# Optimization experiments

Hardware: AMD Instinct MI355X
Metric: run time of the kernel (lower is better)

The kernel has to match this reference:

```python
import jax, jax.numpy as jnp
import numpy as np

BATCH, SEQ = 4, 2048
D_MODEL, D_STATE, D_CONV, HEADDIM = 512, 128, 4, 64
D_INNER = 1024          # expand * d_model
NHEADS = 16             # d_inner / headdim
CONV_DIM = D_INNER + 2 * D_STATE   # 1280 (ngroups=1)
D_IN_PROJ = 2 * D_INNER + 2 * D_STATE + NHEADS  # 2320


def setup_inputs() -> dict:
    key = jax.random.key(0)
    ks = jax.random.split(key, 7)
    x = jax.random.normal(ks[0], (BATCH, SEQ, D_MODEL), jnp.float32)
    norm_weight = jnp.ones((D_MODEL,), jnp.float32)
    in_proj_w = jax.random.normal(ks[1], (D_IN_PROJ, D_MODEL), jnp.float32) * 0.02
    conv_w = jax.random.normal(ks[2], (CONV_DIM, 1, D_CONV), jnp.float32) * 0.2
    conv_b = jnp.zeros((CONV_DIM,), jnp.float32)
    dt_bias = jax.random.normal(ks[3], (NHEADS,), jnp.float32) * 0.1
    A_log = jnp.log(jax.random.uniform(ks[4], (NHEADS,), jnp.float32, 1.0, 16.0))
    D_param = jnp.ones((NHEADS,), jnp.float32)
    gated_norm_weight = jnp.ones((D_INNER,), jnp.float32)
    out_proj_w = jax.random.normal(ks[5], (D_MODEL, D_INNER), jnp.float32) * 0.02
    return dict(x=x, norm_weight=norm_weight, in_proj_w=in_proj_w, conv_w=conv_w,
                conv_b=conv_b, dt_bias=dt_bias, A_log=A_log, D_param=D_param,
                gated_norm_weight=gated_norm_weight, out_proj_w=out_proj_w)


def _rmsnorm(x, w, eps):
    return w * (x * jax.lax.rsqrt(jnp.mean(x * x, axis=-1, keepdims=True) + eps))


def _mamba2_forward(x, norm_weight, in_proj_w, conv_w, conv_b, dt_bias,
                    A_log, D_param, gated_norm_weight, out_proj_w):
    b, l, _ = x.shape
    u = _rmsnorm(x, norm_weight, 1e-6)                       # pre-norm (eps=1e-6)
    zxbcdt = u @ in_proj_w.T                                 # (b,l,2320)
    z = zxbcdt[..., :D_INNER]                                # gate
    xBC = zxbcdt[..., D_INNER:D_INNER + CONV_DIM]            # (b,l,1280)
    dt = zxbcdt[..., D_INNER + CONV_DIM:]                    # (b,l,nheads)
    dt = jax.nn.softplus(dt + dt_bias)

    # causal depthwise conv1d over time + SiLU
    conv = jax.lax.conv_general_dilated(
        xBC.transpose(0, 2, 1), conv_w, window_strides=(1,),
        padding=[(D_CONV - 1, 0)], feature_group_count=CONV_DIM,
        dimension_numbers=('NCH', 'OIH', 'NCH'))
    xBC = jax.nn.silu((conv + conv_b[None, :, None]).transpose(0, 2, 1))

    xs = xBC[..., :D_INNER].reshape(b, l, NHEADS, HEADDIM)   # (b,l,h,p)
    Bmat = xBC[..., D_INNER:D_INNER + D_STATE]               # (b,l,n)
    Cmat = xBC[..., D_INNER + D_STATE:]                      # (b,l,n)

    A = -jnp.exp(A_log)                                      # (h,)
    dA = jnp.exp(dt * A)                                     # (b,l,h)
    dtx = dt[..., None] * xs                                 # (b,l,h,p)

    def step(h, inp):
        dA_t, dtx_t, B_t, C_t = inp                          # (b,h),(b,h,p),(b,n),(b,n)
        h = h * dA_t[..., None, None] + dtx_t[..., None] * B_t[:, None, None, :]
        y = jnp.einsum('bhpn,bn->bhp', h, C_t)
        return h, y

    h0 = jnp.zeros((b, NHEADS, HEADDIM, D_STATE), x.dtype)
    _, ys = jax.lax.scan(step, h0, (dA.transpose(1, 0, 2), dtx.transpose(1, 0, 2, 3),
                                    Bmat.transpose(1, 0, 2), Cmat.transpose(1, 0, 2)))
    y = ys.transpose(1, 0, 2, 3) + xs * D_param[None, None, :, None]  # D skip
    y = y.reshape(b, l, D_INNER)

    y = _rmsnorm(y * jax.nn.silu(z), gated_norm_weight, 1e-5)  # RMSNormGated (eps=1e-5)
    return x + y @ out_proj_w.T                                # residual


def reference(x, norm_weight, in_proj_w, conv_w, conv_b, dt_bias,
              A_log, D_param, gated_norm_weight, out_proj_w):
    return _mamba2_forward(x, norm_weight, in_proj_w, conv_w, conv_b, dt_bias,
                           A_log, D_param, gated_norm_weight, out_proj_w)
```

## Files before the change

kernel.cpp:

```cpp
#include <hip/hip_runtime.h>
#include <cstdint>
#include <cstddef>

#define B_ 4
#define L_ 2048
#define DMODEL 512
#define DINNER 1024
#define DSTATE 128
#define NH 16
#define HD 64
#define CONVDIM 1280
#define NPROJ 2320
#define NPAD 2432
#define ML (B_*L_)
#define Q_ 64
#define NCH 32

typedef __bf16 bf16x8 __attribute__((ext_vector_type(8)));
typedef float f32x4 __attribute__((ext_vector_type(4)));
typedef float f32x16 __attribute__((ext_vector_type(16)));

__device__ __forceinline__ float bf2f(ushort u) {
  union { unsigned int i; float f; } v; v.i = ((unsigned int)u) << 16; return v.f;
}
__device__ __forceinline__ ushort f2bf(float f) {
  union { float f; unsigned int i; } v; v.f = f;
  unsigned int u = v.i;
  unsigned int r = (u + 0x7fffu + ((u >> 16) & 1u)) >> 16;
  return (ushort)r;
}
__device__ __forceinline__ float siluf(float x) { return x / (1.f + __expf(-x)); }

__device__ __forceinline__ void gl_lds16(const void* g, void* l) {
  __builtin_amdgcn_global_load_lds(
      (const __attribute__((address_space(1))) unsigned int*)g,
      (__attribute__((address_space(3))) unsigned int*)l,
      16, 0, 0);
}

__global__ __launch_bounds__(256) void k_cvt(const float* __restrict__ wi, const float* __restrict__ wo,
                                             ushort* __restrict__ oi, ushort* __restrict__ oo) {
  int idx = blockIdx.x * 256 + threadIdx.x;
  const int n1 = NPAD * DMODEL;
  if (idx < n1) {
    int n = idx / DMODEL, k = idx % DMODEL;
    oi[idx] = f2bf((n < NPROJ) ? wi[(size_t)n * DMODEL + k] : 0.f);
  } else {
    int j = idx - n1;
    if (j < DMODEL * DINNER) oo[j] = f2bf(wo[j]);
  }
}

__global__ __launch_bounds__(256) void k_rmsnorm(const float* __restrict__ x, const float* __restrict__ w,
                                                 ushort* __restrict__ u) {
  int row = blockIdx.x * 4 + (threadIdx.x >> 6);
  int lane = threadIdx.x & 63;
  const float* xr = x + (size_t)row * DMODEL + lane * 8;
  float4 a = *(const float4*)xr;
  float4 b = *(const float4*)(xr + 4);
  float ss = a.x*a.x + a.y*a.y + a.z*a.z + a.w*a.w + b.x*b.x + b.y*b.y + b.z*b.z + b.w*b.w;
  ss += __shfl_xor(ss, 1);  ss += __shfl_xor(ss, 2);  ss += __shfl_xor(ss, 4);
  ss += __shfl_xor(ss, 8);  ss += __shfl_xor(ss, 16); ss += __shfl_xor(ss, 32);
  float sc = rsqrtf(ss * (1.f / DMODEL) + 1e-6f);
  const float* wr = w + lane * 8;
  float4 wa = *(const float4*)wr;
  float4 wb = *(const float4*)(wr + 4);
  union { ushort s[8]; int4 v; } o;
  o.s[0] = f2bf(a.x * wa.x * sc); o.s[1] = f2bf(a.y * wa.y * sc);
  o.s[2] = f2bf(a.z * wa.z * sc); o.s[3] = f2bf(a.w * wa.w * sc);
  o.s[4] = f2bf(b.x * wb.x * sc); o.s[5] = f2bf(b.y * wb.y * sc);
  o.s[6] = f2bf(b.z * wb.z * sc); o.s[7] = f2bf(b.w * wb.w * sc);
  *(int4*)(u + (size_t)row * DMODEL + lane * 8) = o.v;
}

template <int EPI, int BM, int BN, int MR, int NR>
__global__ __launch_bounds__(256) void gemm_bt(const ushort* __restrict__ A, const ushort* __restrict__ Bm,
                                               void* __restrict__ Cout, const float* __restrict__ resid,
                                               int M, int N, int K, int gx) {
  constexpr int WM = MR * 32, WN = NR * 32;
  constexpr int WAVES_N = BN / WN;
  constexpr int CH_A = BM / 8, CH_B = BN / 8;
  constexpr int PER_A = CH_A / 4, PER_B = CH_B / 4;
  constexpr int SL = PER_A + PER_B;
  __shared__ __align__(16) ushort lA[2][BM * 64];
  __shared__ __align__(16) ushort lB[2][BN * 64];
  const int nwg = gridDim.x;
  const int cpx = nwg >> 3;
  const int bid = blockIdx.x;
  const int swz = (bid & 7) * cpx + (bid >> 3);
  const int n0 = (swz % gx) * BN, m0 = (swz / gx) * BM;
  const int t = threadIdx.x;
  const int wave = t >> 6, lane = t & 63;
  const int wr = wave / WAVES_N, wc = wave % WAVES_N;
  const int r3 = lane >> 3;
  const int ce = (((lane & 7) ^ r3) << 3);
  const int nt = K >> 6;
  f32x16 acc[MR][NR] = {};
  auto stage = [&](int buf, int k0) {
#pragma unroll
    for (int i = 0; i < PER_A; ++i) {
      int chunk = wave * PER_A + i;
      int row = chunk * 8 + r3;
      gl_lds16(A + (size_t)(m0 + row) * K + k0 + ce, (char*)&lA[buf][0] + chunk * 1024);
    }
#pragma unroll
    for (int i = 0; i < PER_B; ++i) {
      int chunk = wave * PER_B + i;
      int row = chunk * 8 + r3;
      gl_lds16(Bm + (size_t)(n0 + row) * K + k0 + ce, (char*)&lB[buf][0] + chunk * 1024);
    }
  };
  stage(0, 0);
  const int rsel = lane & 31;
  const int khi = (lane >> 5) << 3;
  const int kswz = (lane & 7) << 3;
  for (int kt = 0; kt < nt; ++kt) {
    const int cur = kt & 1;
    if (kt + 1 < nt) {
      stage(cur ^ 1, (kt + 1) << 6);
      if constexpr (SL == 8) asm volatile("s_waitcnt vmcnt(8)" ::: "memory");
      else if constexpr (SL == 6) asm volatile("s_waitcnt vmcnt(6)" ::: "memory");
      else asm volatile("s_waitcnt vmcnt(0)" ::: "memory");
    } else {
      asm volatile("s_waitcnt vmcnt(0)" ::: "memory");
    }
    __builtin_amdgcn_s_barrier();
#pragma unroll
    for (int kk = 0; kk < 64; kk += 16) {
      const int kcol = (kk + khi) ^ kswz;
      bf16x8 af[MR], bfr[NR];
#pragma unroll
      for (int m = 0; m < MR; ++m)
        af[m] = *reinterpret_cast<const bf16x8*>(&lA[cur][(wr * WM + m * 32 + rsel) * 64 + kcol]);
#pragma unroll
      for (int n = 0; n < NR; ++n)
        bfr[n] = *reinterpret_cast<const bf16x8*>(&lB[cur][(wc * WN + n * 32 + rsel) * 64 + kcol]);
#pragma unroll
      for (int m = 0; m < MR; ++m)
#pragma unroll
        for (int n = 0; n < NR; ++n)
          acc[m][n] = __builtin_amdgcn_mfma_f32_32x32x16_bf16(af[m], bfr[n], acc[m][n], 0, 0, 0);
    }
    __builtin_amdgcn_s_barrier();
  }
  const int coln = lane & 31;
  const int rbase = (lane >> 5) << 2;
#pragma unroll
  for (int m = 0; m < MR; ++m) {
#pragma unroll
    for (int n = 0; n < NR; ++n) {
      int gm0 = m0 + wr * WM + m * 32 + rbase;
      int gn = n0 + wc * WN + n * 32 + coln;
#pragma unroll
      for (int r = 0; r < 16; ++r) {
        int gm = gm0 + (r & 3) + 8 * (r >> 2);
        float v = acc[m][n][r];
        if (EPI == 0) {
          ((ushort*)Cout)[(size_t)gm * N + gn] = f2bf(v);
        } else {
          ((float*)Cout)[(size_t)gm * N + gn] = v + resid[(size_t)gm * N + gn];
        }
      }
    }
  }
}

__global__ __launch_bounds__(256) void k_dtcum(const ushort* __restrict__ zx, const float* __restrict__ dt_bias,
                                               const float* __restrict__ A_log, float* __restrict__ dtb,
                                               float* __restrict__ acum) {
  int gid = blockIdx.x * 4 + (threadIdx.x >> 6);
  int lane = threadIdx.x & 63;
  int c = gid & 31, h = (gid >> 5) & 15, b = gid >> 9;
  int row = b * L_ + c * Q_ + lane;
  float raw = bf2f(zx[(size_t)row * NPAD + DINNER + CONVDIM + h]) + dt_bias[h];
  float dtv = raw > 20.f ? raw : log1pf(expf(raw));
  dtb[(size_t)row * NH + h] = dtv;
  float a = dtv * (-__expf(A_log[h]));
#pragma unroll
  for (int d = 1; d < 64; d <<= 1) {
    float o = __shfl_up(a, d);
    if (lane >= d) a += o;
  }
  acum[(size_t)row * NH + h] = a;
}

__global__ __launch_bounds__(256) void k_conv(const ushort* __restrict__ zx, const float* __restrict__ cw,
                                              const float* __restrict__ cb, ushort* __restrict__ out) {
  int t = blockIdx.x * 256 + threadIdx.x;
  int cg = t % 160;
  int rb = t / 160;
  int c0 = cg * 8;
  int l0 = (rb & 255) * 8;
  int b = rb >> 8;
  float w0[8], w1[8], w2[8], w3[8], bias[8];
#pragma unroll
  for (int j = 0; j < 8; ++j) {
    float4 wv = *(const float4*)(cw + (c0 + j) * 4);
    w0[j] = wv.x; w1[j] = wv.y; w2[j] = wv.z; w3[j] = wv.w;
    bias[j] = cb[c0 + j];
  }
  const ushort* base = zx + (size_t)(b * L_ + l0) * NPAD + DINNER + c0;
  ushort* ob = out + (size_t)(b * L_ + l0) * CONVDIM + c0;
  union U8 { int4 v; ushort s[8]; };
  float h0[8], h1[8], h2[8];
  if (l0 >= 3) {
    U8 a, bb, cc;
    a.v  = *(const int4*)(base - 3 * NPAD);
    bb.v = *(const int4*)(base - 2 * NPAD);
    cc.v = *(const int4*)(base - 1 * NPAD);
#pragma unroll
    for (int j = 0; j < 8; ++j) { h0[j] = bf2f(a.s[j]); h1[j] = bf2f(bb.s[j]); h2[j] = bf2f(cc.s[j]); }
  } else {
#pragma unroll
    for (int j = 0; j < 8; ++j) { h0[j] = 0.f; h1[j] = 0.f; h2[j] = 0.f; }
  }
#pragma unroll
  for (int i = 0; i < 8; ++i) {
    U8 xv, ov;
    xv.v = *(const int4*)(base + (size_t)i * NPAD);
#pragma unroll
    for (int j = 0; j < 8; ++j) {
      float xc = bf2f(xv.s[j]);
      float v = w0[j] * h0[j] + w1[j] * h1[j] + w2[j] * h2[j] + w3[j] * xc + bias[j];
      ov.s[j] = f2bf(siluf(v));
      h0[j] = h1[j]; h1[j] = h2[j]; h2[j] = xc;
    }
    *(int4*)(ob + (size_t)i * CONVDIM) = ov.v;
  }
}

__global__ __launch_bounds__(256) void k_state(const ushort* __restrict__ xbc, const float* __restrict__ dtb,
                                               const float* __restrict__ acum, ushort* __restrict__ Sbuf) {
  __shared__ __align__(16) ushort sBTW[128 * 72];
  __shared__ __align__(16) ushort sXT[64 * 72];
  __shared__ float sDt[64], sCum[64];
  const int blk = blockIdx.x;
  const int c = blk & 31, h = (blk >> 5) & 15, b = blk >> 9;
  const int row0 = b * L_ + c * Q_;
  const int tid = threadIdx.x;
  const int wave = tid >> 6, lane = tid & 63;
  if (tid < 64) {
    sDt[tid]  = dtb[(size_t)(row0 + tid) * NH + h];
    sCum[tid] = acum[(size_t)(row0 + tid) * NH + h];
  }
  __syncthreads();
  const float T = sCum[63];
#pragma unroll
  for (int i = 0; i < 4; ++i) {
    int idx = i * 256 + tid;
    int r = idx >> 4, n8 = (idx & 15) * 8;
    union { int4 v; ushort s[8]; } bv;
    bv.v = *(const int4*)(xbc + (size_t)(row0 + r) * CONVDIM + DINNER + n8);
    float w = sDt[r] * __expf(T - sCum[r]);
#pragma unroll
    for (int j = 0; j < 8; ++j)
      sBTW[(n8 + j) * 72 + r] = f2bf(bf2f(bv.s[j]) * w);
  }
#pragma unroll
  for (int i = 0; i < 2; ++i) {
    int idx = i * 256 + tid;
    int r = idx >> 3, p8 = (idx & 7) * 8;
    union { int4 v; ushort s[8]; } xv;
    xv.v = *(const int4*)(xbc + (size_t)(row0 + r) * CONVDIM + h * HD + p8);
#pragma unroll
    for (int j = 0; j < 8; ++j) sXT[(p8 + j) * 72 + r] = xv.s[j];
  }
  __syncthreads();
  const int rsel = lane & 15;
  const int t0 = wave * 16;
  f32x4 sa[8] = {};
#pragma unroll
  for (int k0 = 0; k0 < 64; k0 += 32) {
    int ksel = k0 + ((lane >> 4) << 3);
    bf16x8 af = *(const bf16x8*)&sXT[(t0 + rsel) * 72 + ksel];
#pragma unroll
    for (int n = 0; n < 8; ++n) {
      bf16x8 bf_ = *(const bf16x8*)&sBTW[(n * 16 + rsel) * 72 + ksel];
      sa[n] = __builtin_amdgcn_mfma_f32_16x16x32_bf16(af, bf_, sa[n], 0, 0, 0);
    }
  }
  ushort* Sp = Sbuf + (size_t)((b * NH + h) * NCH + c) * (HD * DSTATE);
  int prow = t0 + ((lane >> 4) << 2);
#pragma unroll
  for (int n = 0; n < 8; ++n) {
    int nc = n * 16 + (lane & 15);
#pragma unroll
    for (int r = 0; r < 4; ++r)
      Sp[(prow + r) * DSTATE + nc] = f2bf(sa[n][r]);
  }
}

__global__ __launch_bounds__(256) void k_scan2(ushort* __restrict__ Sbuf, const float* __restrict__ acum) {
  const int blk = blockIdx.x;
  const int ps = blk & 3, bh = blk >> 2;
  const int b = bh >> 4, h = bh & 15;
  const int off = ps * 2048 + threadIdx.x * 8;
  ushort* base = Sbuf + (size_t)bh * NCH * (HD * DSTATE) + off;
  float alphas[NCH];
#pragma unroll
  for (int c = 0; c < NCH; ++c)
    alphas[c] = __expf(acum[(size_t)(b * L_ + c * Q_ + 63) * NH + h]);
  union U8 { int4 v; ushort s[8]; };
  U8 pf[4];
#pragma unroll
  for (int i = 0; i < 4; ++i) pf[i].v = *(const int4*)(base + (size_t)i * (HD * DSTATE));
  float hreg[8] = {};
  U8 hv;
#pragma unroll
  for (int c = 0; c < NCH; ++c) {
    U8 cur = pf[c & 3];
    if (c + 4 < NCH) pf[c & 3].v = *(const int4*)(base + (size_t)(c + 4) * (HD * DSTATE));
#pragma unroll
    for (int i = 0; i < 8; ++i) hv.s[i] = f2bf(hreg[i]);
    *(int4*)(base + (size_t)c * (HD * DSTATE)) = hv.v;
#pragma unroll
    for (int i = 0; i < 8; ++i) hreg[i] = fmaf(alphas[c], hreg[i], bf2f(cur.s[i]));
  }
}

__global__ __launch_bounds__(256) void k_y(const ushort* __restrict__ xbc, const ushort* __restrict__ Hin,
                                           const float* __restrict__ dtb, const float* __restrict__ acum,
                                           const float* __restrict__ Dp, ushort* __restrict__ yb) {
  __shared__ __align__(16) ushort sC[64 * 136];
  __shared__ __align__(16) ushort sB[64 * 136];
  __shared__ __align__(16) ushort sH[64 * 136];
  __shared__ __align__(16) ushort sXT[64 * 72];
  __shared__ float sDt[64], sCum[64];
  const int blk = blockIdx.x;
  const int c = blk & 31, h = (blk >> 5) & 15, b = blk >> 9;
  const int row0 = b * L_ + c * Q_;
  const int tid = threadIdx.x;
  const int wave = tid >> 6, lane = tid & 63;
  if (tid < 64) {
    sDt[tid]  = dtb[(size_t)(row0 + tid) * NH + h];
    sCum[tid] = acum[(size_t)(row0 + tid) * NH + h];
  }
  const ushort* Hp = Hin + (size_t)((b * NH + h) * NCH + c) * (HD * DSTATE);
#pragma unroll
  for (int i = 0; i < 4; ++i) {
    int idx = i * 256 + tid;
    int r = idx >> 4, n8 = (idx & 15) * 8;
    const ushort* src = xbc + (size_t)(row0 + r) * CONVDIM + DINNER + n8;
    *(int4*)&sB[r * 136 + n8] = *(const int4*)src;
    *(int4*)&sC[r * 136 + n8] = *(const int4*)(src + DSTATE);
    *(int4*)&sH[r * 136 + n8] = *(const int4*)(Hp + (size_t)r * DSTATE + n8);
  }
#pragma unroll
  for (int i = 0; i < 2; ++i) {
    int idx = i * 256 + tid;
    int r = idx >> 3, p8 = (idx & 7) * 8;
    union { int4 v; ushort s[8]; } xv;
    xv.v = *(const int4*)(xbc + (size_t)(row0 + r) * CONVDIM + h * HD + p8);
#pragma unroll
    for (int j = 0; j < 8; ++j) sXT[(p8 + j) * 72 + r] = xv.s[j];
  }
  __syncthreads();
  const int rsel = lane & 15;
  const int t0 = wave * 16;
  f32x4 g[4] = {};
  f32x4 y2[4] = {};
#pragma unroll
  for (int k0 = 0; k0 < 128; k0 += 32) {
    int ksel = k0 + ((lane >> 4) << 3);
    bf16x8 af = *(const bf16x8*)&sC[(t0 + rsel) * 136 + ksel];
#pragma unroll
    for (int s = 0; s < 4; ++s) {
      bf16x8 bf_ = *(const bf16x8*)&sB[(s * 16 + rsel) * 136 + ksel];
      g[s] = __builtin_amdgcn_mfma_f32_16x16x32_bf16(af, bf_, g[s], 0, 0, 0);
      bf16x8 hf = *(const bf16x8*)&sH[(s * 16 + rsel) * 136 + ksel];
      y2[s] = __builtin_amdgcn_mfma_f32_16x16x32_bf16(af, hf, y2[s], 0, 0, 0);
    }
  }
  {
    int trow = t0 + ((lane >> 4) << 2);
#pragma unroll
    for (int s = 0; s < 4; ++s) {
      int sc_ = s * 16 + (lane & 15);
      float dts = sDt[sc_], cums = sCum[sc_];
#pragma unroll
      for (int r = 0; r < 4; ++r) {
        int t2 = trow + r;
        float mv = (sc_ <= t2) ? g[s][r] * dts * __expf(sCum[t2] - cums) : 0.f;
        sC[t2 * 136 + sc_] = f2bf(mv);
      }
    }
  }
  f32x4 yi[4] = {};
#pragma unroll
  for (int k0 = 0; k0 < 64; k0 += 32) {
    int ksel = k0 + ((lane >> 4) << 3);
    bf16x8 af = *(const bf16x8*)&sC[(t0 + rsel) * 136 + ksel];
#pragma unroll
    for (int p = 0; p < 4; ++p) {
      bf16x8 bf_ = *(const bf16x8*)&sXT[(p * 16 + rsel) * 72 + ksel];
      yi[p] = __builtin_amdgcn_mfma_f32_16x16x32_bf16(af, bf_, yi[p], 0, 0, 0);
    }
  }
  const float Dh = Dp[h];
  int trow = t0 + ((lane >> 4) << 2);
#pragma unroll
  for (int p = 0; p < 4; ++p) {
    int pc = p * 16 + (lane & 15);
#pragma unroll
    for (int r = 0; r < 4; ++r) {
      int t2 = trow + r;
      float v = yi[p][r] + __expf(sCum[t2]) * y2[p][r] + Dh * bf2f(sXT[pc * 72 + t2]);
      yb[(size_t)(row0 + t2) * DINNER + h * HD + pc] = f2bf(v);
    }
  }
}

__global__ __launch_bounds__(256) void k_gnorm(const ushort* __restrict__ y, const ushort* __restrict__ zx,
                                               const float* __restrict__ gw, ushort* __restrict__ normed) {
  int row = blockIdx.x * 4 + (threadIdx.x >> 6);
  int lane = threadIdx.x & 63;
  int j0 = lane * 16;
  const ushort* yr = y + (size_t)row * DINNER + j0;
  union { int4 v; ushort s[8]; } y0, y1;
  y0.v = *(const int4*)yr;
  y1.v = *(const int4*)(yr + 8);
  const ushort* zr = zx + (size_t)row * NPAD + j0;
  union { int4 v; ushort s[8]; } z0, z1;
  z0.v = *(const int4*)zr;
  z1.v = *(const int4*)(zr + 8);
  float yg[16];
  float ss = 0.f;
#pragma unroll
  for (int i = 0; i < 8; ++i) {
    float g = bf2f(y0.s[i]) * siluf(bf2f(z0.s[i]));
    yg[i] = g; ss += g * g;
  }
#pragma unroll
  for (int i = 0; i < 8; ++i) {
    float g = bf2f(y1.s[i]) * siluf(bf2f(z1.s[i]));
    yg[8 + i] = g; ss += g * g;
  }
  ss += __shfl_xor(ss, 1);  ss += __shfl_xor(ss, 2);  ss += __shfl_xor(ss, 4);
  ss += __shfl_xor(ss, 8);  ss += __shfl_xor(ss, 16); ss += __shfl_xor(ss, 32);
  float sc = rsqrtf(ss * (1.f / DINNER) + 1e-5f);
  float gwv[16];
#pragma unroll
  for (int i = 0; i < 4; ++i) *(float4*)&gwv[i * 4] = *(const float4*)(gw + j0 + i * 4);
  union { int4 v; ushort s[8]; } o0, o1;
#pragma unroll
  for (int i = 0; i < 8; ++i) o0.s[i] = f2bf(yg[i] * sc * gwv[i]);
#pragma unroll
  for (int i = 0; i < 8; ++i) o1.s[i] = f2bf(yg[8 + i] * sc * gwv[8 + i]);
  ushort* op = normed + (size_t)row * DINNER + j0;
  *(int4*)op = o0.v;
  *(int4*)(op + 8) = o1.v;
}

extern "C" void kernel_launch(void* const* d_in, const int* in_sizes, int n_in,
                              void* d_out, int out_size, void* d_ws, size_t ws_size,
                              hipStream_t stream) {
  const float* x         = (const float*)d_in[0];
  const float* norm_w    = (const float*)d_in[1];
  const float* in_proj_w = (const float*)d_in[2];
  const float* conv_w    = (const float*)d_in[3];
  const float* conv_b    = (const float*)d_in[4];
  const float* dt_bias   = (const float*)d_in[5];
  const float* A_log     = (const float*)d_in[6];
  const float* D_param   = (const float*)d_in[7];
  const float* gnw       = (const float*)d_in[8];
  const float* out_proj_w= (const float*)d_in[9];

  char* ws = (char*)d_ws;
  ushort* u      = (ushort*)(ws + 0);
  ushort* Wb     = (ushort*)(ws + 8388608);
  ushort* Woutb  = (ushort*)(ws + 10878976);
  float*  dtb    = (float*)(ws + 11927552);
  float*  acum   = (float*)(ws + 12451840);
  ushort* zx     = (ushort*)(ws + 12976128);
  ushort* convo  = (ushort*)(ws + 52822016);
  ushort* yb     = (ushort*)(ws + 73793536);
  ushort* Sbuf   = (ushort*)(ws + 90570752);
  ushort* normed = convo;

  k_cvt<<<(NPAD * DMODEL + DMODEL * DINNER + 255) / 256, 256, 0, stream>>>(in_proj_w, out_proj_w, Wb, Woutb);
  k_rmsnorm<<<ML / 4, 256, 0, stream>>>(x, norm_w, u);
  gemm_bt<0, 128, 128, 2, 2><<<(NPAD / 128) * (ML / 128), 256, 0, stream>>>(u, Wb, (void*)zx, nullptr, ML, NPAD, DMODEL, NPAD / 128);
  k_dtcum<<<512, 256, 0, stream>>>(zx, dt_bias, A_log, dtb, acum);
  k_conv<<<640, 256, 0, stream>>>(zx, conv_w, conv_b, convo);
  k_state<<<2048, 256, 0, stream>>>(convo, dtb, acum, Sbuf);
  k_scan2<<<256, 256, 0, stream>>>(Sbuf, acum);
  k_y<<<2048, 256, 0, stream>>>(convo, Sbuf, dtb, acum, D_param, yb);
  k_gnorm<<<ML / 4, 256, 0, stream>>>(yb, zx, gnw, normed);
  gemm_bt<1, 128, 64, 2, 1><<<(DMODEL / 64) * (ML / 128), 256, 0, stream>>>(normed, Woutb, d_out, x, ML, DMODEL, DINNER, DMODEL / 64);
}
```

Before: 151.9 us.

## Split GEMM tile staging to overlap B-tile loads with mid-tile MFMA compute

Result: slower. 160.8 us (+5.8%).

```diff
diff --git a/kernel.cpp b/kernel.cpp
--- a/kernel.cpp
+++ b/kernel.cpp
@@ -81,7 +81,6 @@
   constexpr int WAVES_N = BN / WN;
   constexpr int CH_A = BM / 8, CH_B = BN / 8;
   constexpr int PER_A = CH_A / 4, PER_B = CH_B / 4;
-  constexpr int SL = PER_A + PER_B;
   __shared__ __align__(16) ushort lA[2][BM * 64];
   __shared__ __align__(16) ushort lB[2][BN * 64];
   const int nwg = gridDim.x;
@@ -96,13 +95,15 @@
   const int ce = (((lane & 7) ^ r3) << 3);
   const int nt = K >> 6;
   f32x16 acc[MR][NR] = {};
-  auto stage = [&](int buf, int k0) {
+  auto stageA = [&](int buf, int k0) {
 #pragma unroll
     for (int i = 0; i < PER_A; ++i) {
       int chunk = wave * PER_A + i;
       int row = chunk * 8 + r3;
       gl_lds16(A + (size_t)(m0 + row) * K + k0 + ce, (char*)&lA[buf][0] + chunk * 1024);
     }
+  };
+  auto stageB = [&](int buf, int k0) {
 #pragma unroll
     for (int i = 0; i < PER_B; ++i) {
       int chunk = wave * PER_B + i;
@@ -110,23 +111,25 @@
       gl_lds16(Bm + (size_t)(n0 + row) * K + k0 + ce, (char*)&lB[buf][0] + chunk * 1024);
     }
   };
-  stage(0, 0);
+  stageA(0, 0);
+  stageB(0, 0);
   const int rsel = lane & 31;
   const int khi = (lane >> 5) << 3;
   const int kswz = (lane & 7) << 3;
   for (int kt = 0; kt < nt; ++kt) {
     const int cur = kt & 1;
     if (kt + 1 < nt) {
-      stage(cur ^ 1, (kt + 1) << 6);
-      if constexpr (SL == 8) asm volatile("s_waitcnt vmcnt(8)" ::: "memory");
-      else if constexpr (SL == 6) asm volatile("s_waitcnt vmcnt(6)" ::: "memory");
+      stageA(cur ^ 1, (kt + 1) << 6);
+      if constexpr (PER_A == 4) asm volatile("s_waitcnt vmcnt(4)" ::: "memory");
+      else if constexpr (PER_A == 2) asm volatile("s_waitcnt vmcnt(2)" ::: "memory");
       else asm volatile("s_waitcnt vmcnt(0)" ::: "memory");
     } else {
       asm volatile("s_waitcnt vmcnt(0)" ::: "memory");
     }
     __builtin_amdgcn_s_barrier();
-#pragma unroll
-    for (int kk = 0; kk < 64; kk += 16) {
+    __builtin_amdgcn_s_setprio(1);
+#pragma unroll
+    for (int kk = 0; kk < 32; kk += 16) {
       const int kcol = (kk + khi) ^ kswz;
       bf16x8 af[MR], bfr[NR];
 #pragma unroll
@@ -141,6 +144,27 @@
         for (int n = 0; n < NR; ++n)
           acc[m][n] = __builtin_amdgcn_mfma_f32_32x32x16_bf16(af[m], bfr[n], acc[m][n], 0, 0, 0);
     }
+    __builtin_amdgcn_s_setprio(0);
+    if (kt + 1 < nt) stageB(cur ^ 1, (kt + 1) << 6);
+    __builtin_amdgcn_s_barrier();
+    __builtin_amdgcn_s_setprio(1);
+#pragma unroll
+    for (int kk = 32; kk < 64; kk += 16) {
+      const int kcol = (kk + khi) ^ kswz;
+      bf16x8 af[MR], bfr[NR];
+#pragma unroll
+      for (int m = 0; m < MR; ++m)
+        af[m] = *reinterpret_cast<const bf16x8*>(&lA[cur][(wr * WM + m * 32 + rsel) * 64 + kcol]);
+#pragma unroll
+      for (int n = 0; n < NR; ++n)
+        bfr[n] = *reinterpret_cast<const bf16x8*>(&lB[cur][(wc * WN + n * 32 + rsel) * 64 + kcol]);
+#pragma unroll
+      for (int m = 0; m < MR; ++m)
+#pragma unroll
+        for (int n = 0; n < NR; ++n)
+          acc[m][n] = __builtin_amdgcn_mfma_f32_32x32x16_bf16(af[m], bfr[n], acc[m][n], 0, 0, 0);
+    }
+    __builtin_amdgcn_s_setprio(0);
     __builtin_amdgcn_s_barrier();
   }
   const int coln = lane & 31;
```

## Fuse gated RMSNorm into y kernel and output GEMM epilogue

Applied to the files above, without the earlier changes.

New measurement: 149.3 us. About the same (-1.8%).

```diff
diff --git a/kernel.cpp b/kernel.cpp
--- a/kernel.cpp
+++ b/kernel.cpp
@@ -39,6 +39,7 @@
 }
 
 __global__ __launch_bounds__(256) void k_cvt(const float* __restrict__ wi, const float* __restrict__ wo,
+                                             const float* __restrict__ gw,
                                              ushort* __restrict__ oi, ushort* __restrict__ oo) {
   int idx = blockIdx.x * 256 + threadIdx.x;
   const int n1 = NPAD * DMODEL;
@@ -47,7 +48,7 @@
     oi[idx] = f2bf((n < NPROJ) ? wi[(size_t)n * DMODEL + k] : 0.f);
   } else {
     int j = idx - n1;
-    if (j < DMODEL * DINNER) oo[j] = f2bf(wo[j]);
+    if (j < DMODEL * DINNER) oo[j] = f2bf(wo[j] * gw[j & (DINNER - 1)]);
   }
 }
 
@@ -76,6 +77,7 @@
 template <int EPI, int BM, int BN, int MR, int NR>
 __global__ __launch_bounds__(256) void gemm_bt(const ushort* __restrict__ A, const ushort* __restrict__ Bm,
                                                void* __restrict__ Cout, const float* __restrict__ resid,
+                                               const float* __restrict__ rescale,
                                                int M, int N, int K, int gx) {
   constexpr int WM = MR * 32, WN = NR * 32;
   constexpr int WAVES_N = BN / WN;
@@ -158,7 +160,7 @@
         if (EPI == 0) {
           ((ushort*)Cout)[(size_t)gm * N + gn] = f2bf(v);
         } else {
-          ((float*)Cout)[(size_t)gm * N + gn] = v + resid[(size_t)gm * N + gn];
+          ((float*)Cout)[(size_t)gm * N + gn] = v * rescale[gm] + resid[(size_t)gm * N + gn];
         }
       }
     }
@@ -167,7 +169,9 @@
 
 __global__ __launch_bounds__(256) void k_dtcum(const ushort* __restrict__ zx, const float* __restrict__ dt_bias,
                                                const float* __restrict__ A_log, float* __restrict__ dtb,
-                                               float* __restrict__ acum) {
+                                               float* __restrict__ acum, float* __restrict__ rs) {
+  int flat = blockIdx.x * 256 + threadIdx.x;
+  if (flat < ML) rs[flat] = 0.f;
   int gid = blockIdx.x * 4 + (threadIdx.x >> 6);
   int lane = threadIdx.x & 63;
   int c = gid & 31, h = (gid >> 5) & 15, b = gid >> 9;
@@ -318,9 +322,11 @@
   }
 }
 
-__global__ __launch_bounds__(256) void k_y(const ushort* __restrict__ xbc, const ushort* __restrict__ Hin,
+__global__ __launch_bounds__(256) void k_y(const ushort* __restrict__ xbc, const ushort* __restrict__ zx,
+                                           const ushort* __restrict__ Hin,
                                            const float* __restrict__ dtb, const float* __restrict__ acum,
-                                           const float* __restrict__ Dp, ushort* __restrict__ yb) {
+                                           const float* __restrict__ Dp, ushort* __restrict__ yb,
+                                           float* __restrict__ rs) {
   __shared__ __align__(16) ushort sC[64 * 136];
   __shared__ __align__(16) ushort sB[64 * 136];
   __shared__ __align__(16) ushort sH[64 * 136];
@@ -398,6 +404,7 @@
   }
   const float Dh = Dp[h];
   int trow = t0 + ((lane >> 4) << 2);
+  float rsum[4] = {0.f, 0.f, 0.f, 0.f};
 #pragma unroll
   for (int p = 0; p < 4; ++p) {
     int pc = p * 16 + (lane & 15);
@@ -405,50 +412,23 @@
     for (int r = 0; r < 4; ++r) {
       int t2 = trow + r;
       float v = yi[p][r] + __expf(sCum[t2]) * y2[p][r] + Dh * bf2f(sXT[pc * 72 + t2]);
-      yb[(size_t)(row0 + t2) * DINNER + h * HD + pc] = f2bf(v);
-    }
-  }
-}
-
-__global__ __launch_bounds__(256) void k_gnorm(const ushort* __restrict__ y, const ushort* __restrict__ zx,
-                                               const float* __restrict__ gw, ushort* __restrict__ normed) {
-  int row = blockIdx.x * 4 + (threadIdx.x >> 6);
-  int lane = threadIdx.x & 63;
-  int j0 = lane * 16;
-  const ushort* yr = y + (size_t)row * DINNER + j0;
-  union { int4 v; ushort s[8]; } y0, y1;
-  y0.v = *(const int4*)yr;
-  y1.v = *(const int4*)(yr + 8);
-  const ushort* zr = zx + (size_t)row * NPAD + j0;
-  union { int4 v; ushort s[8]; } z0, z1;
-  z0.v = *(const int4*)zr;
-  z1.v = *(const int4*)(zr + 8);
-  float yg[16];
-  float ss = 0.f;
-#pragma unroll
-  for (int i = 0; i < 8; ++i) {
-    float g = bf2f(y0.s[i]) * siluf(bf2f(z0.s[i]));
-    yg[i] = g; ss += g * g;
-  }
-#pragma unroll
-  for (int i = 0; i < 8; ++i) {
-    float g = bf2f(y1.s[i]) * siluf(bf2f(z1.s[i]));
-    yg[8 + i] = g; ss += g * g;
-  }
-  ss += __shfl_xor(ss, 1);  ss += __shfl_xor(ss, 2);  ss += __shfl_xor(ss, 4);
-  ss += __shfl_xor(ss, 8);  ss += __shfl_xor(ss, 16); ss += __shfl_xor(ss, 32);
-  float sc = rsqrtf(ss * (1.f / DINNER) + 1e-5f);
-  float gwv[16];
-#pragma unroll
-  for (int i = 0; i < 4; ++i) *(float4*)&gwv[i * 4] = *(const float4*)(gw + j0 + i * 4);
-  union { int4 v; ushort s[8]; } o0, o1;
-#pragma unroll
-  for (int i = 0; i < 8; ++i) o0.s[i] = f2bf(yg[i] * sc * gwv[i]);
-#pragma unroll
-  for (int i = 0; i < 8; ++i) o1.s[i] = f2bf(yg[8 + i] * sc * gwv[8 + i]);
-  ushort* op = normed + (size_t)row * DINNER + j0;
-  *(int4*)op = o0.v;
-  *(int4*)(op + 8) = o1.v;
+      float zf = bf2f(zx[(size_t)(row0 + t2) * NPAD + h * HD + pc]);
+      float gg = v * siluf(zf);
+      rsum[r] += gg * gg;
+      yb[(size_t)(row0 + t2) * DINNER + h * HD + pc] = f2bf(gg);
+    }
+  }
+#pragma unroll
+  for (int r = 0; r < 4; ++r) {
+    float s = rsum[r];
+    s += __shfl_xor(s, 1); s += __shfl_xor(s, 2); s += __shfl_xor(s, 4); s += __shfl_xor(s, 8);
+    if ((lane & 15) == 0) atomicAdd(&rs[row0 + trow + r], s);
+  }
+}
+
+__global__ __launch_bounds__(256) void k_scale(float* __restrict__ rs) {
+  int i = blockIdx.x * 256 + threadIdx.x;
+  rs[i] = rsqrtf(rs[i] * (1.f / DINNER) + 1e-5f);
 }
 
 extern "C" void kernel_launch(void* const* d_in, const int* in_sizes, int n_in,
@@ -467,6 +447,7 @@
 
   char* ws = (char*)d_ws;
   ushort* u      = (ushort*)(ws + 0);
+  float*  rs     = (float*)(ws + 0);
   ushort* Wb     = (ushort*)(ws + 8388608);
   ushort* Woutb  = (ushort*)(ws + 10878976);
   float*  dtb    = (float*)(ws + 11927552);
@@ -475,16 +456,15 @@
   ushort* convo  = (ushort*)(ws + 52822016);
   ushort* yb     = (ushort*)(ws + 73793536);
   ushort* Sbuf   = (ushort*)(ws + 90570752);
-  ushort* normed = convo;
-
-  k_cvt<<<(NPAD * DMODEL + DMODEL * DINNER + 255) / 256, 256, 0, stream>>>(in_proj_w, out_proj_w, Wb, Woutb);
+
+  k_cvt<<<(NPAD * DMODEL + DMODEL * DINNER + 255) / 256, 256, 0, stream>>>(in_proj_w, out_proj_w, gnw, Wb, Woutb);
   k_rmsnorm<<<ML / 4, 256, 0, stream>>>(x, norm_w, u);
-  gemm_bt<0, 128, 128, 2, 2><<<(NPAD / 128) * (ML / 128), 256, 0, stream>>>(u, Wb, (void*)zx, nullptr, ML, NPAD, DMODEL, NPAD / 128);
-  k_dtcum<<<512, 256, 0, stream>>>(zx, dt_bias, A_log, dtb, acum);
+  gemm_bt<0, 128, 128, 2, 2><<<(NPAD / 128) * (ML / 128), 256, 0, stream>>>(u, Wb, (void*)zx, nullptr, nullptr, ML, NPAD, DMODEL, NPAD / 128);
+  k_dtcum<<<512, 256, 0, stream>>>(zx, dt_bias, A_log, dtb, acum, rs);
   k_conv<<<640, 256, 0, stream>>>(zx, conv_w, conv_b, convo);
   k_state<<<2048, 256, 0, stream>>>(convo, dtb, acum, Sbuf);
   k_scan2<<<256, 256, 0, stream>>>(Sbuf, acum);
-  k_y<<<2048, 256, 0, stream>>>(convo, Sbuf, dtb, acum, D_param, yb);
-  k_gnorm<<<ML / 4, 256, 0, stream>>>(yb, zx, gnw, normed);
-  gemm_bt<1, 128, 64, 2, 1><<<(DMODEL / 64) * (ML / 128), 256, 0, stream>>>(normed, Woutb, d_out, x, ML, DMODEL, DINNER, DMODEL / 64);
-}
+  k_y<<<2048, 256, 0, stream>>>(convo, zx, Sbuf, dtb, acum, D_param, yb, rs);
+  k_scale<<<ML / 256, 256, 0, stream>>>(rs);
+  gemm_bt<3, 128, 64, 2, 1><<<(DMODEL / 64) * (ML / 128), 256, 0, stream>>>(yb, Woutb, d_out, x, rs, ML, DMODEL, DINNER, DMODEL / 64);
+}
```
